# Kernel tuning notes

Measured on AMD Instinct MI355X. Metric: run time of the kernel, lower is better.

Reference implementation:

```python
import jax, jax.numpy as jnp
import numpy as np

TIME_WINDOW = 100  # init arg: time_window
RATIO = 1.0        # init arg: ratio


def setup_inputs() -> dict:
    key = jax.random.key(0)
    img = jax.random.uniform(key, (16, 1, 224, 224), dtype=jnp.float32)  # values in [0,1)
    return {"img": img}


def reference(img):
    T = TIME_WINDOW
    orig_shape = img.shape
    N = img.size
    flat = img.reshape(-1) * RATIO                      # [N]
    nz = flat != 0
    # rate = 1/(img*ratio) where nonzero, else 0 (Poisson(0) samples are always 0)
    lam = jnp.where(nz, 1.0 / jnp.where(nz, flat, 1.0), 0.0)
    key = jax.random.key(42)
    intervals = jax.random.poisson(key, lam, shape=(T, N)).astype(jnp.float32)  # [T, N]
    # for nonzero pixels, force a minimum inter-spike interval of 1 timestep
    intervals = jnp.where(nz[None, :] & (intervals == 0), 1.0, intervals)
    times = jnp.cumsum(intervals, axis=0).astype(jnp.int32)  # [T, N], spike times >= 1
    # times beyond the window collapse into row 0 (discarded below)
    times = jnp.where(times >= T + 1, 0, times)
    spikes = jnp.zeros((T + 1, N), dtype=bool)
    col = jnp.arange(N, dtype=jnp.int32)
    spikes = spikes.at[times, col[None, :]].set(True)   # scatter by computed times
    spikes = spikes[1:]                                  # drop the dump row 0
    return spikes.reshape((T,) + orig_shape)
```

## Files before the change

### kernel.cpp

```cpp
#include <hip/hip_runtime.h>
#include <math.h>
#include <stdint.h>

#pragma clang fp contract(off)

#define N_PIX 802816
#define T_WIN 100
#define KN_MAX 96
#define RJ_MAX 48
#define G_SLOT (KN_MAX * 2 + RJ_MAX * 4)
#define TAB_BASE 98000
#define TAB_N    4096
#define TAB_WS   (G_SLOT + 1)
#define WS_NEEDED ((TAB_WS + TAB_N) * 4)

__device__ __forceinline__ void tf2x32(uint32_t k0, uint32_t k1,
                                       uint32_t x0, uint32_t x1,
                                       uint32_t &o0, uint32_t &o1) {
  uint32_t ks2 = k0 ^ k1 ^ 0x1BD11BDAu;
  x0 += k0; x1 += k1;
#define TF_R(r) { x0 += x1; x1 = (x1 << (r)) | (x1 >> (32 - (r))); x1 ^= x0; }
  TF_R(13) TF_R(15) TF_R(26) TF_R(6)
  x0 += k1;  x1 += ks2 + 1u;
  TF_R(17) TF_R(29) TF_R(16) TF_R(24)
  x0 += ks2; x1 += k0 + 2u;
  TF_R(13) TF_R(15) TF_R(26) TF_R(6)
  x0 += k0;  x1 += k1 + 3u;
  TF_R(17) TF_R(29) TF_R(16) TF_R(24)
  x0 += k1;  x1 += ks2 + 4u;
  TF_R(13) TF_R(15) TF_R(26) TF_R(6)
  x0 += ks2; x1 += k0 + 5u;
#undef TF_R
  o0 = x0; o1 = x1;
}

__device__ __forceinline__ uint32_t unif_bits(uint32_t s0, uint32_t s1, uint32_t p) {
  uint32_t a, b;
  tf2x32(s0, s1, 0u, p, a, b);
  return a ^ b;
}

__device__ __forceinline__ float bits_to_unit(uint32_t bits) {
  return __uint_as_float(0x3f800000u | (bits >> 9)) - 1.0f;
}

__device__ __forceinline__ float xla_logf(float xin) {
#pragma clang fp contract(off)
  if (xin == 0.0f) return __uint_as_float(0xff800000u);
  if (!(xin > 0.0f)) return __uint_as_float(0x7fc00000u);
  float x = fmaxf(xin, __uint_as_float(0x00800000u));
  uint32_t ib = __float_as_uint(x);
  float e = (float)((int)(ib >> 23) - 126);
  ib = (ib & 0x007fffffu) | 0x3f000000u;
  x = __uint_as_float(ib);
  float tmp = 0.0f, eadj = 0.0f;
  if (x < (float)0.707106781186547524) { tmp = x; eadj = 1.0f; }
  x = x - 1.0f;
  e = e - eadj;
  x = x + tmp;
  float x2 = x * x;
  float x3 = x2 * x;
  float y  = fmaf((float)7.0376836292e-2,  x, (float)-1.1514610310e-1);
  float y1 = fmaf((float)-1.2420140846e-1, x, (float)1.4249322787e-1);
  float y2 = fmaf((float)2.0000714765e-1,  x, (float)-2.4999993993e-1);
  y  = fmaf(y,  x, (float)1.1676998740e-1);
  y1 = fmaf(y1, x, (float)-1.6668057665e-1);
  y2 = fmaf(y2, x, (float)3.3333331174e-1);
  y  = fmaf(y, x3, y1);
  y  = fmaf(y, x3, y2);
  float eq1 = e * (float)-2.12194440e-4;
  y = fmaf(y, x3, eq1);
  x = fmaf(-x2, 0.5f, x);
  x = x + y;
  x = fmaf(e, (float)0.693359375, x);
  return x;
}

__device__ __forceinline__ float xla_log1pf(float w) {
#pragma clang fp contract(off)
  if (fabsf(w) < (float)1e-4) return fmaf(-0.5f, w, 1.0f) * w;
  return xla_logf(w + 1.0f);
}

__device__ __forceinline__ float xla_lgammaf_pos(float x) {
#pragma clang fp contract(off)
  const float kBase = (float)0.99999999999980993227684700473478;
  const float c0 = (float)676.520368121885098567009190444019;
  const float c1 = (float)-1259.13921672240287047156078755283;
  const float c2 = (float)771.3234287776530788486528258894;
  const float c3 = (float)-176.61502916214059906584551354;
  const float c4 = (float)12.507343278686904814458936853;
  const float c5 = (float)-0.13857109526572011689554707;
  const float c6 = (float)9.984369578019570859563e-6;
  const float c7 = (float)1.50563273514931155834e-7;
  const float kLogSqrtTwoPi = (float)0.91893853320467274178032973640562;
  const float kGPlusHalf = 7.5f;
  const float kLogGPlusHalf = (float)2.0149030205422647065;
  float z = x - 1.0f;
  float sum = kBase;
  sum = sum + c0 / ((z + 0.0f) + 1.0f);
  sum = sum + c1 / ((z + 1.0f) + 1.0f);
  sum = sum + c2 / ((z + 2.0f) + 1.0f);
  sum = sum + c3 / ((z + 3.0f) + 1.0f);
  sum = sum + c4 / ((z + 4.0f) + 1.0f);
  sum = sum + c5 / ((z + 5.0f) + 1.0f);
  sum = sum + c6 / ((z + 6.0f) + 1.0f);
  sum = sum + c7 / ((z + 7.0f) + 1.0f);
  float t = kGPlusHalf + z;
  float log_t = kLogGPlusHalf + xla_log1pf(z / kGPlusHalf);
  float log_y = fmaf((z + 0.5f) - t / log_t, log_t, kLogSqrtTwoPi) + xla_logf(sum);
  return log_y;
}

struct RejConst {
  float lam, neg_lam, log_lam, aa, bb, inv_alpha, v_r, two_a;
};

__device__ __forceinline__ RejConst make_rej(float lam) {
  RejConst rc;
  rc.lam = lam;
  rc.neg_lam = -lam;
  rc.log_lam = xla_logf(lam);
  float sq = (float)sqrt((double)lam);
  rc.bb = fmaf(2.53f, sq, (float)0.931);
  rc.aa = fmaf((float)0.02483, rc.bb, (float)-0.059);
  rc.inv_alpha = (float)1.1239 + (float)1.1328 / (rc.bb - (float)3.4);
  rc.v_r = (float)0.9277 - (float)3.6224 / (rc.bb - 2.0f);
  rc.two_a = 2.0f * rc.aa;
  return rc;
}

__device__ __forceinline__ bool rej_step4(const RejConst& rc, uint4 ch,
                                          uint32_t p, float& kf_out) {
  float u = bits_to_unit(unif_bits(ch.x, ch.y, p)) - 0.5f;
  float v = bits_to_unit(unif_bits(ch.z, ch.w, p));
  float u_sh = 0.5f - fabsf(u);
  float kf = floorf(fmaf(rc.two_a / u_sh + rc.bb, u, rc.lam) + (float)0.43);
  kf_out = kf;
  if ((u_sh >= (float)0.07) && (v <= rc.v_r)) return true;
  if ((kf < 0.0f) || ((u_sh < (float)0.013) && (v > u_sh))) return false;
  float sv = xla_logf((v * rc.inv_alpha) / ((rc.aa / (u_sh * u_sh)) + rc.bb));
  float tv = fmaf(kf, rc.log_lam, rc.neg_lam) - xla_lgammaf_pos(kf + 1.0f);
  return sv <= tv;
}

__global__ void chain_init(uint32_t* __restrict__ ws, int build_table) {
  if (blockIdx.x == 0) {
    if (threadIdx.x != 0) return;
    ws[G_SLOT] = 0u;
    uint32_t r0 = 0u, r1 = 42u;
    for (int j = 0; j < KN_MAX; ++j) {
      uint32_t s0, s1, n0, n1;
      tf2x32(r0, r1, 0u, 1u, s0, s1);
      tf2x32(r0, r1, 0u, 0u, n0, n1);
      ws[2 * j] = s0; ws[2 * j + 1] = s1;
      r0 = n0; r1 = n1;
    }
  } else if (blockIdx.x == 1) {
    if (threadIdx.x != 0) return;
    uint32_t c0 = 0u, c1 = 42u;
    for (int j = 0; j < RJ_MAX; ++j) {
      uint32_t a0, a1, b0, b1, n0, n1;
      tf2x32(c0, c1, 0u, 1u, a0, a1);
      tf2x32(c0, c1, 0u, 2u, b0, b1);
      tf2x32(c0, c1, 0u, 0u, n0, n1);
      uint32_t base = KN_MAX * 2 + 4 * j;
      ws[base + 0] = a0; ws[base + 1] = a1; ws[base + 2] = b0; ws[base + 3] = b1;
      c0 = n0; c1 = n1;
    }
  } else if (build_table) {
    int i = (blockIdx.x - 2) * 256 + threadIdx.x;
    if (i < TAB_N) {
      float kf = (float)(TAB_BASE + i);
      ws[TAB_WS + i] = __float_as_uint(xla_lgammaf_pos(kf + 1.0f));
    }
  }
}

__global__ void __launch_bounds__(512)
rej_gmax(const float* __restrict__ img, const uint32_t* __restrict__ ws,
         uint32_t* __restrict__ gmax, int use_table) {
  __shared__ uint4 rj4[RJ_MAX];
  __shared__ float lgtab[TAB_N];
  __shared__ int waveRej[8];
  __shared__ unsigned short order[512];
  __shared__ uint32_t red[512];

  const int tid = threadIdx.x;
  for (int i = tid; i < RJ_MAX; i += 512) {
    uint32_t b = KN_MAX * 2 + 4 * i;
    rj4[i] = make_uint4(ws[b], ws[b + 1], ws[b + 2], ws[b + 3]);
  }
  if (use_table)
    for (int i = tid; i < TAB_N; i += 512) lgtab[i] = __uint_as_float(ws[TAB_WS + i]);

  int n0 = blockIdx.x * 512 + tid;
  float uimg0 = img[n0];
  bool isRej = (uimg0 != 0.0f) && !((1.0f / uimg0) < 10.0f);
  int lane = tid & 63, w = tid >> 6;
  unsigned long long bal = __ballot(isRej ? 1 : 0);
  int within = (int)__popcll(bal & ((1ull << lane) - 1ull));
  if (lane == 0) waveRej[w] = (int)__popcll(bal);
  __syncthreads();
  int rejBefore = 0, totalRej = 0;
  for (int i = 0; i < 8; ++i) { int c = waveRej[i]; totalRej += c; if (i < w) rejBefore += c; }
  int nMasked = 512 - totalRej;
  int slot = isRej ? (nMasked + rejBefore + within)
                   : (64 * w - rejBefore) + (lane - within);
  order[slot] = (unsigned short)tid;
  __syncthreads();

  int n = blockIdx.x * 512 + (int)order[tid];
  bool myRej = (tid >= nMasked);
  RejConst rc = make_rej(myRej ? (1.0f / img[n]) : 100000.0f);

  uint32_t mymax = 1;
  {
    uint32_t p = (uint32_t)n;
    int t = 0, j = 0;
    while (t < T_WIN) {
      uint4 ch = rj4[j];
      float u = bits_to_unit(unif_bits(ch.x, ch.y, p)) - 0.5f;
      float v = bits_to_unit(unif_bits(ch.z, ch.w, p));
      float u_sh = 0.5f - fabsf(u);
      float kf = floorf(fmaf(rc.two_a / u_sh + rc.bb, u, rc.lam) + (float)0.43);
      bool acc;
      if ((u_sh >= (float)0.07) && (v <= rc.v_r)) acc = true;
      else if ((kf < 0.0f) || ((u_sh < (float)0.013) && (v > u_sh))) acc = false;
      else {
        float sv = xla_logf((v * rc.inv_alpha) / ((rc.aa / (u_sh * u_sh)) + rc.bb));
        int ki = (int)kf - TAB_BASE;
        float lg;
        if (use_table && ki >= 0 && ki < TAB_N) lg = lgtab[ki];
        else lg = xla_lgammaf_pos(kf + 1.0f);
        float tv = fmaf(kf, rc.log_lam, rc.neg_lam) - lg;
        acc = (sv <= tv);
      }
      if (acc) {
        uint32_t fa = (uint32_t)(j + 1);
        if (fa > mymax) mymax = fa;
        ++t; p += N_PIX; j = 0;
      } else if (++j >= RJ_MAX) {
        mymax = RJ_MAX;
        ++t; p += N_PIX; j = 0;
      }
    }
  }
  red[tid] = mymax;
  __syncthreads();
  for (int s2 = 256; s2 > 0; s2 >>= 1) {
    if (tid < s2) {
      uint32_t o = red[tid + s2];
      if (o > red[tid]) red[tid] = o;
    }
    __syncthreads();
  }
  if (tid == 0) atomicMax((unsigned int*)gmax, red[0]);
}

__global__ void __launch_bounds__(512)
spike_main(const float* __restrict__ img, int* __restrict__ out,
           const uint32_t* __restrict__ chains) {
  __shared__ uint2 kn2[KN_MAX];
  __shared__ uint4 rj4[RJ_MAX];
  __shared__ int waveRej[8];
  __shared__ unsigned short order[512];
  __shared__ int shG;
  __shared__ ulonglong2 bmsh[512];

  const int tid = threadIdx.x;
  for (int i = tid; i < KN_MAX; i += 512)
    kn2[i] = make_uint2(chains[2 * i], chains[2 * i + 1]);
  for (int i = tid; i < RJ_MAX; i += 512) {
    uint32_t b = KN_MAX * 2 + 4 * i;
    rj4[i] = make_uint4(chains[b], chains[b + 1], chains[b + 2], chains[b + 3]);
  }
  if (tid == 0) shG = (int)chains[G_SLOT];

  int n0 = blockIdx.x * 512 + tid;
  float uimg0 = img[n0];
  bool isRej = (uimg0 != 0.0f) && !((1.0f / uimg0) < 10.0f);
  int lane = tid & 63, w = tid >> 6;
  unsigned long long bal = __ballot(isRej ? 1 : 0);
  int within = (int)__popcll(bal & ((1ull << lane) - 1ull));
  if (lane == 0) waveRej[w] = (int)__popcll(bal);
  __syncthreads();
  int rejBefore = 0, totalRej = 0;
  for (int i = 0; i < 8; ++i) { int c = waveRej[i]; totalRej += c; if (i < w) rejBefore += c; }
  int nMasked = 512 - totalRej;
  int slot = isRej ? (nMasked + rejBefore + within)
                   : (64 * w - rejBefore) + (lane - within);
  order[slot] = (unsigned short)tid;
  __syncthreads();

  const int G = shG;
  int nl = (int)order[tid];
  int n = blockIdx.x * 512 + nl;
  bool myRej = (tid >= nMasked);
  float uimg = img[n];
  unsigned long long bm0 = 0ull, bm1 = 0ull;

  if (myRej) {
    RejConst rc = make_rej(1.0f / uimg);
    uint32_t p = (uint32_t)n;
    int s = 0, j = G - 1, t = 0;
    while (t < T_WIN) {
      float kf;
      bool acc = rej_step4(rc, rj4[j], p, kf);
      if (acc) {
        int iv = (kf >= 102.0f) ? 102 : (int)kf;
        if (iv == 0) iv = 1;
        s += iv;
        if (s > T_WIN) break;
        if (s <= 64) bm0 |= 1ull << (s - 1); else bm1 |= 1ull << (s - 65);
        ++t; p += N_PIX; j = G - 1;
      } else if (--j < 0) {
        break;
      }
    }
  } else if (uimg != 0.0f) {
    float lam = 1.0f / uimg;
    float neg_lam = -lam;
    uint32_t p = (uint32_t)n;
    int s = 0, k = 0, j = 0;
    float lp = 0.0f;
    while (true) {
      uint2 sk = kn2[j];
      float u = bits_to_unit(unif_bits(sk.x, sk.y, p));
      ++k; ++j;
      lp = lp + xla_logf(u);
      if (lp <= neg_lam || j >= KN_MAX) {
        int iv = k - 1;
        if (iv == 0) iv = 1;
        s += iv;
        if (s > T_WIN) break;
        if (s <= 64) bm0 |= 1ull << (s - 1); else bm1 |= 1ull << (s - 65);
        p += N_PIX; j = 0; k = 0; lp = 0.0f;
        if (p >= (uint32_t)T_WIN * (uint32_t)N_PIX) break;
      }
    }
  }

  ulonglong2 bm; bm.x = bm0; bm.y = bm1;
  bmsh[nl] = bm;
  __syncthreads();
  ulonglong2 b2 = bmsh[tid];
  size_t base = (size_t)(blockIdx.x * 512 + tid);
  for (int t = 0; t < 64; ++t)
    out[base + (size_t)t * N_PIX] = (int)((b2.x >> t) & 1ull);
  for (int t = 64; t < T_WIN; ++t)
    out[base + (size_t)t * N_PIX] = (int)((b2.y >> (t - 64)) & 1ull);
}

extern "C" void kernel_launch(void* const* d_in, const int* in_sizes, int n_in,
                              void* d_out, int out_size, void* d_ws, size_t ws_size,
                              hipStream_t stream) {
  const float* img = (const float*)d_in[0];
  int* out = (int*)d_out;
  uint32_t* ws = (uint32_t*)d_ws;
  int use_table = (ws_size >= (size_t)WS_NEEDED) ? 1 : 0;
  hipLaunchKernelGGL(chain_init, dim3(2 + TAB_N / 256), dim3(256), 0, stream,
                     ws, use_table);
  hipLaunchKernelGGL(rej_gmax, dim3(N_PIX / 512), dim3(512), 0, stream,
                     img, ws, ws + G_SLOT, use_table);
  hipLaunchKernelGGL(spike_main, dim3(N_PIX / 512), dim3(512), 0, stream,
                     img, out, ws);
}
```

Baseline: 1.243 ms.

## Split rejection max-chain search into first-candidate pass plus compacted retry list

The single rej_gmax kernel becomes two stages. A first pass evaluates only the first rejection candidate for every pixel and timestep and appends the rejected (pixel, timestep) positions to a global list through wave-local buffers and atomics. A second kernel grid-strides over that list only, walking the rest of the chain to find the global maximum chain length. The old full kernel stays as a fallback that runs only on list overflow or when the workspace is too small. The aim is to remove the divergence and serial while-loop cost of the old per-pixel walk. In exchange it needs a 32 MB list, global atomics and two extra launches.

```diff
diff --git a/kernel.cpp b/kernel.cpp
--- a/kernel.cpp
+++ b/kernel.cpp
@@ -9,10 +9,17 @@
 #define KN_MAX 96
 #define RJ_MAX 48
 #define G_SLOT (KN_MAX * 2 + RJ_MAX * 4)
+#define MRC_WS (G_SLOT + 1)
+#define CNT_WS (MRC_WS + 8)
+#define OVF_WS (CNT_WS + 1)
 #define TAB_BASE 98000
 #define TAB_N    4096
-#define TAB_WS   (G_SLOT + 1)
-#define WS_NEEDED ((TAB_WS + TAB_N) * 4)
+#define TAB_WS   (OVF_WS + 1)
+#define LIST_WS  (TAB_WS + TAB_N)
+#define LIST_CAP (8u * 1024u * 1024u)
+#define WS_TAB_NEEDED ((size_t)(TAB_WS + TAB_N) * 4)
+#define WS_FAST_NEEDED ((size_t)(LIST_WS + LIST_CAP) * 4)
+#define WBUF 640
 
 __device__ __forceinline__ void tf2x32(uint32_t k0, uint32_t k1,
                                        uint32_t x0, uint32_t x1,
@@ -144,10 +151,28 @@
   return sv <= tv;
 }
 
-__global__ void chain_init(uint32_t* __restrict__ ws, int build_table) {
+__device__ __forceinline__ bool rej_step_tab(const RejConst& rc, uint4 ch,
+                                             uint32_t p, const float* lgtab,
+                                             float& kf_out) {
+  float u = bits_to_unit(unif_bits(ch.x, ch.y, p)) - 0.5f;
+  float v = bits_to_unit(unif_bits(ch.z, ch.w, p));
+  float u_sh = 0.5f - fabsf(u);
+  float kf = floorf(fmaf(rc.two_a / u_sh + rc.bb, u, rc.lam) + (float)0.43);
+  kf_out = kf;
+  if ((u_sh >= (float)0.07) && (v <= rc.v_r)) return true;
+  if ((kf < 0.0f) || ((u_sh < (float)0.013) && (v > u_sh))) return false;
+  float sv = xla_logf((v * rc.inv_alpha) / ((rc.aa / (u_sh * u_sh)) + rc.bb));
+  int ki = (int)kf - TAB_BASE;
+  float lg = (ki >= 0 && ki < TAB_N) ? lgtab[ki] : xla_lgammaf_pos(kf + 1.0f);
+  float tv = fmaf(kf, rc.log_lam, rc.neg_lam) - lg;
+  return sv <= tv;
+}
+
+__global__ void chain_init(uint32_t* __restrict__ ws, int build_table, int fast) {
   if (blockIdx.x == 0) {
     if (threadIdx.x != 0) return;
-    ws[G_SLOT] = 0u;
+    ws[G_SLOT] = 1u;
+    if (fast) { ws[CNT_WS] = 0u; ws[OVF_WS] = 0u; }
     uint32_t r0 = 0u, r1 = 42u;
     for (int j = 0; j < KN_MAX; ++j) {
       uint32_t s0, s1, n0, n1;
@@ -157,16 +182,27 @@
       r0 = n0; r1 = n1;
     }
   } else if (blockIdx.x == 1) {
-    if (threadIdx.x != 0) return;
-    uint32_t c0 = 0u, c1 = 42u;
-    for (int j = 0; j < RJ_MAX; ++j) {
-      uint32_t a0, a1, b0, b1, n0, n1;
-      tf2x32(c0, c1, 0u, 1u, a0, a1);
-      tf2x32(c0, c1, 0u, 2u, b0, b1);
-      tf2x32(c0, c1, 0u, 0u, n0, n1);
-      uint32_t base = KN_MAX * 2 + 4 * j;
-      ws[base + 0] = a0; ws[base + 1] = a1; ws[base + 2] = b0; ws[base + 3] = b1;
-      c0 = n0; c1 = n1;
+    if (threadIdx.x == 0) {
+      uint32_t c0 = 0u, c1 = 42u;
+      for (int j = 0; j < RJ_MAX; ++j) {
+        uint32_t a0, a1, b0, b1, n0, n1;
+        tf2x32(c0, c1, 0u, 1u, a0, a1);
+        tf2x32(c0, c1, 0u, 2u, b0, b1);
+        tf2x32(c0, c1, 0u, 0u, n0, n1);
+        uint32_t base = KN_MAX * 2 + 4 * j;
+        ws[base + 0] = a0; ws[base + 1] = a1; ws[base + 2] = b0; ws[base + 3] = b1;
+        c0 = n0; c1 = n1;
+      }
+    } else if (threadIdx.x == 64 && fast) {
+      RejConst m = make_rej(100000.0f);
+      ws[MRC_WS + 0] = __float_as_uint(m.lam);
+      ws[MRC_WS + 1] = __float_as_uint(m.neg_lam);
+      ws[MRC_WS + 2] = __float_as_uint(m.log_lam);
+      ws[MRC_WS + 3] = __float_as_uint(m.aa);
+      ws[MRC_WS + 4] = __float_as_uint(m.bb);
+      ws[MRC_WS + 5] = __float_as_uint(m.inv_alpha);
+      ws[MRC_WS + 6] = __float_as_uint(m.v_r);
+      ws[MRC_WS + 7] = __float_as_uint(m.two_a);
     }
   } else if (build_table) {
     int i = (blockIdx.x - 2) * 256 + threadIdx.x;
@@ -177,22 +213,25 @@
   }
 }
 
+__device__ __forceinline__ RejConst load_mrc(const float* mrcsh) {
+  RejConst rc;
+  rc.lam = mrcsh[0]; rc.neg_lam = mrcsh[1]; rc.log_lam = mrcsh[2];
+  rc.aa = mrcsh[3];  rc.bb = mrcsh[4];      rc.inv_alpha = mrcsh[5];
+  rc.v_r = mrcsh[6]; rc.two_a = mrcsh[7];
+  return rc;
+}
+
 __global__ void __launch_bounds__(512)
-rej_gmax(const float* __restrict__ img, const uint32_t* __restrict__ ws,
-         uint32_t* __restrict__ gmax, int use_table) {
-  __shared__ uint4 rj4[RJ_MAX];
+rej_pass0(const float* __restrict__ img, uint32_t* __restrict__ ws) {
   __shared__ float lgtab[TAB_N];
+  __shared__ float mrcsh[8];
   __shared__ int waveRej[8];
   __shared__ unsigned short order[512];
-  __shared__ uint32_t red[512];
+  __shared__ uint32_t wbuf[8][WBUF];
 
   const int tid = threadIdx.x;
-  for (int i = tid; i < RJ_MAX; i += 512) {
-    uint32_t b = KN_MAX * 2 + 4 * i;
-    rj4[i] = make_uint4(ws[b], ws[b + 1], ws[b + 2], ws[b + 3]);
-  }
-  if (use_table)
-    for (int i = tid; i < TAB_N; i += 512) lgtab[i] = __uint_as_float(ws[TAB_WS + i]);
+  for (int i = tid; i < TAB_N; i += 512) lgtab[i] = __uint_as_float(ws[TAB_WS + i]);
+  if (tid < 8) mrcsh[tid] = __uint_as_float(ws[MRC_WS + tid]);
 
   int n0 = blockIdx.x * 512 + tid;
   float uimg0 = img[n0];
@@ -212,6 +251,132 @@
 
   int n = blockIdx.x * 512 + (int)order[tid];
   bool myRej = (tid >= nMasked);
+  RejConst rc;
+  if (myRej) rc = make_rej(1.0f / img[n]);
+  else       rc = load_mrc(mrcsh);
+
+  uint4 ch0 = make_uint4(ws[KN_MAX * 2 + 0], ws[KN_MAX * 2 + 1],
+                         ws[KN_MAX * 2 + 2], ws[KN_MAX * 2 + 3]);
+  uint32_t* cnt  = ws + CNT_WS;
+  uint32_t* list = ws + LIST_WS;
+  uint32_t wcnt = 0;
+  uint32_t p = (uint32_t)n;
+
+  for (int t = 0; t < T_WIN; ++t, p += N_PIX) {
+    float kf;
+    bool acc = rej_step_tab(rc, ch0, p, lgtab, kf);
+    unsigned long long mask = __ballot(acc ? 0 : 1);
+    if (mask) {
+      uint32_t rank = (uint32_t)__popcll(mask & ((1ull << lane) - 1ull));
+      if (!acc) wbuf[w][wcnt + rank] = p;
+      wcnt += (uint32_t)__popcll(mask);
+    }
+    if (wcnt >= WBUF - 64) {
+      uint32_t base = 0;
+      if (lane == 0) base = atomicAdd(cnt, wcnt);
+      base = (uint32_t)__shfl((int)base, 0, 64);
+      for (uint32_t i = (uint32_t)lane; i < wcnt; i += 64) {
+        uint32_t idx = base + i;
+        if (idx < LIST_CAP) list[idx] = wbuf[w][i];
+        else atomicOr(ws + OVF_WS, 1u);
+      }
+      wcnt = 0;
+    }
+  }
+  if (wcnt > 0) {
+    uint32_t base = 0;
+    if (lane == 0) base = atomicAdd(cnt, wcnt);
+    base = (uint32_t)__shfl((int)base, 0, 64);
+    for (uint32_t i = (uint32_t)lane; i < wcnt; i += 64) {
+      uint32_t idx = base + i;
+      if (idx < LIST_CAP) list[idx] = wbuf[w][i];
+      else atomicOr(ws + OVF_WS, 1u);
+    }
+  }
+}
+
+__global__ void __launch_bounds__(256)
+rej_finish(const float* __restrict__ img, uint32_t* __restrict__ ws,
+           uint32_t* __restrict__ gmax) {
+  __shared__ uint4 rj4[RJ_MAX];
+  __shared__ float lgtab[TAB_N];
+  __shared__ float mrcsh[8];
+  __shared__ uint32_t red[256];
+  const int tid = threadIdx.x;
+  for (int i = tid; i < RJ_MAX; i += 256) {
+    uint32_t b = KN_MAX * 2 + 4 * i;
+    rj4[i] = make_uint4(ws[b], ws[b + 1], ws[b + 2], ws[b + 3]);
+  }
+  for (int i = tid; i < TAB_N; i += 256) lgtab[i] = __uint_as_float(ws[TAB_WS + i]);
+  if (tid < 8) mrcsh[tid] = __uint_as_float(ws[MRC_WS + tid]);
+  __syncthreads();
+
+  uint32_t cnt = ws[CNT_WS];
+  if (cnt > LIST_CAP) cnt = LIST_CAP;
+  uint32_t mymax = 1;
+  for (uint32_t i = blockIdx.x * 256 + tid; i < cnt; i += gridDim.x * 256) {
+    uint32_t p = ws[LIST_WS + i];
+    uint32_t n = p % (uint32_t)N_PIX;
+    float uimg = img[n];
+    bool isRej = (uimg != 0.0f) && !((1.0f / uimg) < 10.0f);
+    RejConst rc;
+    if (isRej) rc = make_rej(1.0f / uimg);
+    else       rc = load_mrc(mrcsh);
+    uint32_t fa = RJ_MAX;
+    for (int j = 1; j < RJ_MAX; ++j) {
+      float kf;
+      if (rej_step_tab(rc, rj4[j], p, lgtab, kf)) { fa = (uint32_t)(j + 1); break; }
+    }
+    if (fa > mymax) mymax = fa;
+  }
+  red[tid] = mymax;
+  __syncthreads();
+  for (int s2 = 128; s2 > 0; s2 >>= 1) {
+    if (tid < s2) {
+      uint32_t o = red[tid + s2];
+      if (o > red[tid]) red[tid] = o;
+    }
+    __syncthreads();
+  }
+  if (tid == 0) atomicMax((unsigned int*)gmax, red[0]);
+}
+
+__global__ void __launch_bounds__(512)
+rej_gmax_full(const float* __restrict__ img, const uint32_t* __restrict__ ws,
+              uint32_t* __restrict__ gmax, int use_table, int skip_unless_ovf) {
+  if (skip_unless_ovf && ws[OVF_WS] == 0u) return;
+  __shared__ uint4 rj4[RJ_MAX];
+  __shared__ float lgtab[TAB_N];
+  __shared__ int waveRej[8];
+  __shared__ unsigned short order[512];
+  __shared__ uint32_t red[512];
+
+  const int tid = threadIdx.x;
+  for (int i = tid; i < RJ_MAX; i += 512) {
+    uint32_t b = KN_MAX * 2 + 4 * i;
+    rj4[i] = make_uint4(ws[b], ws[b + 1], ws[b + 2], ws[b + 3]);
+  }
+  if (use_table)
+    for (int i = tid; i < TAB_N; i += 512) lgtab[i] = __uint_as_float(ws[TAB_WS + i]);
+
+  int n0 = blockIdx.x * 512 + tid;
+  float uimg0 = img[n0];
+  bool isRej = (uimg0 != 0.0f) && !((1.0f / uimg0) < 10.0f);
+  int lane = tid & 63, w = tid >> 6;
+  unsigned long long bal = __ballot(isRej ? 1 : 0);
+  int within = (int)__popcll(bal & ((1ull << lane) - 1ull));
+  if (lane == 0) waveRej[w] = (int)__popcll(bal);
+  __syncthreads();
+  int rejBefore = 0, totalRej = 0;
+  for (int i = 0; i < 8; ++i) { int c = waveRej[i]; totalRej += c; if (i < w) rejBefore += c; }
+  int nMasked = 512 - totalRej;
+  int slot = isRej ? (nMasked + rejBefore + within)
+                   : (64 * w - rejBefore) + (lane - within);
+  order[slot] = (unsigned short)tid;
+  __syncthreads();
+
+  int n = blockIdx.x * 512 + (int)order[tid];
+  bool myRej = (tid >= nMasked);
   RejConst rc = make_rej(myRej ? (1.0f / img[n]) : 100000.0f);
 
   uint32_t mymax = 1;
@@ -219,23 +384,10 @@
     uint32_t p = (uint32_t)n;
     int t = 0, j = 0;
     while (t < T_WIN) {
-      uint4 ch = rj4[j];
-      float u = bits_to_unit(unif_bits(ch.x, ch.y, p)) - 0.5f;
-      float v = bits_to_unit(unif_bits(ch.z, ch.w, p));
-      float u_sh = 0.5f - fabsf(u);
-      float kf = floorf(fmaf(rc.two_a / u_sh + rc.bb, u, rc.lam) + (float)0.43);
+      float kf;
       bool acc;
-      if ((u_sh >= (float)0.07) && (v <= rc.v_r)) acc = true;
-      else if ((kf < 0.0f) || ((u_sh < (float)0.013) && (v > u_sh))) acc = false;
-      else {
-        float sv = xla_logf((v * rc.inv_alpha) / ((rc.aa / (u_sh * u_sh)) + rc.bb));
-        int ki = (int)kf - TAB_BASE;
-        float lg;
-        if (use_table && ki >= 0 && ki < TAB_N) lg = lgtab[ki];
-        else lg = xla_lgammaf_pos(kf + 1.0f);
-        float tv = fmaf(kf, rc.log_lam, rc.neg_lam) - lg;
-        acc = (sv <= tv);
-      }
+      if (use_table) acc = rej_step_tab(rc, rj4[j], p, lgtab, kf);
+      else           acc = rej_step4(rc, rj4[j], p, kf);
       if (acc) {
         uint32_t fa = (uint32_t)(j + 1);
         if (fa > mymax) mymax = fa;
@@ -358,11 +510,18 @@
   const float* img = (const float*)d_in[0];
   int* out = (int*)d_out;
   uint32_t* ws = (uint32_t*)d_ws;
-  int use_table = (ws_size >= (size_t)WS_NEEDED) ? 1 : 0;
+  int use_table = (ws_size >= WS_TAB_NEEDED) ? 1 : 0;
+  int use_fast  = (use_table && ws_size >= WS_FAST_NEEDED) ? 1 : 0;
+
   hipLaunchKernelGGL(chain_init, dim3(2 + TAB_N / 256), dim3(256), 0, stream,
-                     ws, use_table);
-  hipLaunchKernelGGL(rej_gmax, dim3(N_PIX / 512), dim3(512), 0, stream,
-                     img, ws, ws + G_SLOT, use_table);
+                     ws, use_table, use_fast);
+  if (use_fast) {
+    hipLaunchKernelGGL(rej_pass0, dim3(N_PIX / 512), dim3(512), 0, stream, img, ws);
+    hipLaunchKernelGGL(rej_finish, dim3(512), dim3(256), 0, stream,
+                       img, ws, ws + G_SLOT);
+  }
+  hipLaunchKernelGGL(rej_gmax_full, dim3(N_PIX / 512), dim3(512), 0, stream,
+                     img, ws, ws + G_SLOT, use_table, use_fast);
   hipLaunchKernelGGL(spike_main, dim3(N_PIX / 512), dim3(512), 0, stream,
                      img, out, ws);
 }
```

Result: slower. 2.565 ms (+106.3%).

## Use persistent blocks with atomic chunk work-stealing for gmax and spike kernels

Applied to the files above, without the earlier changes.

Both the rejection-max kernel and the spike kernel become persistent grids of 1024 blocks that pull 512-pixel chunks from global atomic counters instead of one block per chunk. This is meant to balance the uneven per-chunk cost of rejection sampling and to amortize the per-block setup of the chain tables and lgamma LDS table. It adds an atomic plus two barriers per chunk and a fallback kernel for when the workspace is too small. The G slot now starts at 1 and is clamped.

```diff
diff --git a/kernel.cpp b/kernel.cpp
--- a/kernel.cpp
+++ b/kernel.cpp
@@ -8,11 +8,15 @@
 #define T_WIN 100
 #define KN_MAX 96
 #define RJ_MAX 48
-#define G_SLOT (KN_MAX * 2 + RJ_MAX * 4)
+#define N_CHUNK 1568
+
+#define G_SLOT 384
+#define CTR0_WS 385
+#define CTR1_WS 386
+#define TAB_WS  400
 #define TAB_BASE 98000
 #define TAB_N    4096
-#define TAB_WS   (G_SLOT + 1)
-#define WS_NEEDED ((TAB_WS + TAB_N) * 4)
+#define WS_TAB_NEEDED ((size_t)(TAB_WS + TAB_N) * 4)
 
 __device__ __forceinline__ void tf2x32(uint32_t k0, uint32_t k1,
                                        uint32_t x0, uint32_t x1,
@@ -144,10 +148,28 @@
   return sv <= tv;
 }
 
+__device__ __forceinline__ bool rej_step_lds(const RejConst& rc, uint4 ch,
+                                             uint32_t p, const float* lgtab,
+                                             float& kf_out) {
+  float u = bits_to_unit(unif_bits(ch.x, ch.y, p)) - 0.5f;
+  float v = bits_to_unit(unif_bits(ch.z, ch.w, p));
+  float u_sh = 0.5f - fabsf(u);
+  float kf = floorf(fmaf(rc.two_a / u_sh + rc.bb, u, rc.lam) + (float)0.43);
+  kf_out = kf;
+  if ((u_sh >= (float)0.07) && (v <= rc.v_r)) return true;
+  if ((kf < 0.0f) || ((u_sh < (float)0.013) && (v > u_sh))) return false;
+  float sv = xla_logf((v * rc.inv_alpha) / ((rc.aa / (u_sh * u_sh)) + rc.bb));
+  int ki = (int)kf - TAB_BASE;
+  float lg = (ki >= 0 && ki < TAB_N) ? lgtab[ki] : xla_lgammaf_pos(kf + 1.0f);
+  float tv = fmaf(kf, rc.log_lam, rc.neg_lam) - lg;
+  return sv <= tv;
+}
+
 __global__ void chain_init(uint32_t* __restrict__ ws, int build_table) {
   if (blockIdx.x == 0) {
     if (threadIdx.x != 0) return;
-    ws[G_SLOT] = 0u;
+    ws[G_SLOT] = 1u;
+    ws[CTR0_WS] = 0u; ws[CTR1_WS] = 0u;
     uint32_t r0 = 0u, r1 = 42u;
     for (int j = 0; j < KN_MAX; ++j) {
       uint32_t s0, s1, n0, n1;
@@ -178,64 +200,56 @@
 }
 
 __global__ void __launch_bounds__(512)
-rej_gmax(const float* __restrict__ img, const uint32_t* __restrict__ ws,
-         uint32_t* __restrict__ gmax, int use_table) {
+gmax_ws(const float* __restrict__ img, uint32_t* __restrict__ ws,
+        uint32_t* __restrict__ gmax) {
   __shared__ uint4 rj4[RJ_MAX];
   __shared__ float lgtab[TAB_N];
   __shared__ int waveRej[8];
   __shared__ unsigned short order[512];
   __shared__ uint32_t red[512];
+  __shared__ uint32_t curC;
 
   const int tid = threadIdx.x;
   for (int i = tid; i < RJ_MAX; i += 512) {
     uint32_t b = KN_MAX * 2 + 4 * i;
     rj4[i] = make_uint4(ws[b], ws[b + 1], ws[b + 2], ws[b + 3]);
   }
-  if (use_table)
-    for (int i = tid; i < TAB_N; i += 512) lgtab[i] = __uint_as_float(ws[TAB_WS + i]);
-
-  int n0 = blockIdx.x * 512 + tid;
-  float uimg0 = img[n0];
-  bool isRej = (uimg0 != 0.0f) && !((1.0f / uimg0) < 10.0f);
-  int lane = tid & 63, w = tid >> 6;
-  unsigned long long bal = __ballot(isRej ? 1 : 0);
-  int within = (int)__popcll(bal & ((1ull << lane) - 1ull));
-  if (lane == 0) waveRej[w] = (int)__popcll(bal);
-  __syncthreads();
-  int rejBefore = 0, totalRej = 0;
-  for (int i = 0; i < 8; ++i) { int c = waveRej[i]; totalRej += c; if (i < w) rejBefore += c; }
-  int nMasked = 512 - totalRej;
-  int slot = isRej ? (nMasked + rejBefore + within)
-                   : (64 * w - rejBefore) + (lane - within);
-  order[slot] = (unsigned short)tid;
-  __syncthreads();
-
-  int n = blockIdx.x * 512 + (int)order[tid];
-  bool myRej = (tid >= nMasked);
-  RejConst rc = make_rej(myRej ? (1.0f / img[n]) : 100000.0f);
+  for (int i = tid; i < TAB_N; i += 512)
+    lgtab[i] = __uint_as_float(ws[TAB_WS + i]);
 
   uint32_t mymax = 1;
-  {
+  while (true) {
+    __syncthreads();
+    if (tid == 0) curC = atomicAdd(ws + CTR0_WS, 1u);
+    __syncthreads();
+    uint32_t c = curC;
+    if (c >= (uint32_t)N_CHUNK) break;
+
+    int n0 = (int)c * 512 + tid;
+    float uimg0 = img[n0];
+    bool isRej = (uimg0 != 0.0f) && !((1.0f / uimg0) < 10.0f);
+    int lane = tid & 63, w = tid >> 6;
+    unsigned long long bal = __ballot(isRej ? 1 : 0);
+    int within = (int)__popcll(bal & ((1ull << lane) - 1ull));
+    if (lane == 0) waveRej[w] = (int)__popcll(bal);
+    __syncthreads();
+    int rejBefore = 0, totalRej = 0;
+    for (int i = 0; i < 8; ++i) { int cc = waveRej[i]; totalRej += cc; if (i < w) rejBefore += cc; }
+    int nMasked = 512 - totalRej;
+    int slot = isRej ? (nMasked + rejBefore + within)
+                     : (64 * w - rejBefore) + (lane - within);
+    order[slot] = (unsigned short)tid;
+    __syncthreads();
+
+    int n = (int)c * 512 + (int)order[tid];
+    bool myRej = (tid >= nMasked);
+    RejConst rc = make_rej(myRej ? (1.0f / img[n]) : 100000.0f);
+
     uint32_t p = (uint32_t)n;
     int t = 0, j = 0;
     while (t < T_WIN) {
-      uint4 ch = rj4[j];
-      float u = bits_to_unit(unif_bits(ch.x, ch.y, p)) - 0.5f;
-      float v = bits_to_unit(unif_bits(ch.z, ch.w, p));
-      float u_sh = 0.5f - fabsf(u);
-      float kf = floorf(fmaf(rc.two_a / u_sh + rc.bb, u, rc.lam) + (float)0.43);
-      bool acc;
-      if ((u_sh >= (float)0.07) && (v <= rc.v_r)) acc = true;
-      else if ((kf < 0.0f) || ((u_sh < (float)0.013) && (v > u_sh))) acc = false;
-      else {
-        float sv = xla_logf((v * rc.inv_alpha) / ((rc.aa / (u_sh * u_sh)) + rc.bb));
-        int ki = (int)kf - TAB_BASE;
-        float lg;
-        if (use_table && ki >= 0 && ki < TAB_N) lg = lgtab[ki];
-        else lg = xla_lgammaf_pos(kf + 1.0f);
-        float tv = fmaf(kf, rc.log_lam, rc.neg_lam) - lg;
-        acc = (sv <= tv);
-      }
+      float kf;
+      bool acc = rej_step_lds(rc, rj4[j], p, lgtab, kf);
       if (acc) {
         uint32_t fa = (uint32_t)(j + 1);
         if (fa > mymax) mymax = fa;
@@ -246,6 +260,7 @@
       }
     }
   }
+
   red[tid] = mymax;
   __syncthreads();
   for (int s2 = 256; s2 > 0; s2 >>= 1) {
@@ -259,14 +274,57 @@
 }
 
 __global__ void __launch_bounds__(512)
-spike_main(const float* __restrict__ img, int* __restrict__ out,
-           const uint32_t* __restrict__ chains) {
+rej_gmax_full(const float* __restrict__ img, const uint32_t* __restrict__ ws,
+              uint32_t* __restrict__ gmax) {
+  __shared__ uint4 rj4[RJ_MAX];
+  __shared__ uint32_t red[512];
+  const int tid = threadIdx.x;
+  for (int i = tid; i < RJ_MAX; i += 512) {
+    uint32_t b = KN_MAX * 2 + 4 * i;
+    rj4[i] = make_uint4(ws[b], ws[b + 1], ws[b + 2], ws[b + 3]);
+  }
+  __syncthreads();
+  int n = blockIdx.x * 512 + tid;
+  float uimg = img[n];
+  bool isRej = (uimg != 0.0f) && !((1.0f / uimg) < 10.0f);
+  RejConst rc = make_rej(isRej ? (1.0f / uimg) : 100000.0f);
+  uint32_t mymax = 1;
+  uint32_t p = (uint32_t)n;
+  int t = 0, j = 0;
+  while (t < T_WIN) {
+    float kf;
+    bool acc = rej_step4(rc, rj4[j], p, kf);
+    if (acc) {
+      uint32_t fa = (uint32_t)(j + 1);
+      if (fa > mymax) mymax = fa;
+      ++t; p += N_PIX; j = 0;
+    } else if (++j >= RJ_MAX) {
+      mymax = RJ_MAX;
+      ++t; p += N_PIX; j = 0;
+    }
+  }
+  red[tid] = mymax;
+  __syncthreads();
+  for (int s2 = 256; s2 > 0; s2 >>= 1) {
+    if (tid < s2) {
+      uint32_t o = red[tid + s2];
+      if (o > red[tid]) red[tid] = o;
+    }
+    __syncthreads();
+  }
+  if (tid == 0) atomicMax((unsigned int*)gmax, red[0]);
+}
+
+__global__ void __launch_bounds__(512)
+spike_ws(const float* __restrict__ img, int* __restrict__ out,
+         const uint32_t* __restrict__ chains, uint32_t* __restrict__ wsctr) {
   __shared__ uint2 kn2[KN_MAX];
   __shared__ uint4 rj4[RJ_MAX];
   __shared__ int waveRej[8];
   __shared__ unsigned short order[512];
   __shared__ int shG;
   __shared__ ulonglong2 bmsh[512];
+  __shared__ uint32_t curC;
 
   const int tid = threadIdx.x;
   for (int i = tid; i < KN_MAX; i += 512)
@@ -275,81 +333,94 @@
     uint32_t b = KN_MAX * 2 + 4 * i;
     rj4[i] = make_uint4(chains[b], chains[b + 1], chains[b + 2], chains[b + 3]);
   }
-  if (tid == 0) shG = (int)chains[G_SLOT];
-
-  int n0 = blockIdx.x * 512 + tid;
-  float uimg0 = img[n0];
-  bool isRej = (uimg0 != 0.0f) && !((1.0f / uimg0) < 10.0f);
-  int lane = tid & 63, w = tid >> 6;
-  unsigned long long bal = __ballot(isRej ? 1 : 0);
-  int within = (int)__popcll(bal & ((1ull << lane) - 1ull));
-  if (lane == 0) waveRej[w] = (int)__popcll(bal);
-  __syncthreads();
-  int rejBefore = 0, totalRej = 0;
-  for (int i = 0; i < 8; ++i) { int c = waveRej[i]; totalRej += c; if (i < w) rejBefore += c; }
-  int nMasked = 512 - totalRej;
-  int slot = isRej ? (nMasked + rejBefore + within)
-                   : (64 * w - rejBefore) + (lane - within);
-  order[slot] = (unsigned short)tid;
-  __syncthreads();
-
-  const int G = shG;
-  int nl = (int)order[tid];
-  int n = blockIdx.x * 512 + nl;
-  bool myRej = (tid >= nMasked);
-  float uimg = img[n];
-  unsigned long long bm0 = 0ull, bm1 = 0ull;
-
-  if (myRej) {
-    RejConst rc = make_rej(1.0f / uimg);
-    uint32_t p = (uint32_t)n;
-    int s = 0, j = G - 1, t = 0;
-    while (t < T_WIN) {
-      float kf;
-      bool acc = rej_step4(rc, rj4[j], p, kf);
-      if (acc) {
-        int iv = (kf >= 102.0f) ? 102 : (int)kf;
-        if (iv == 0) iv = 1;
-        s += iv;
-        if (s > T_WIN) break;
-        if (s <= 64) bm0 |= 1ull << (s - 1); else bm1 |= 1ull << (s - 65);
-        ++t; p += N_PIX; j = G - 1;
-      } else if (--j < 0) {
-        break;
+  if (tid == 0) {
+    int g = (int)chains[G_SLOT];
+    if (g < 1) g = 1;
+    if (g > RJ_MAX) g = RJ_MAX;
+    shG = g;
+  }
+
+  while (true) {
+    __syncthreads();
+    if (tid == 0) curC = atomicAdd(wsctr, 1u);
+    __syncthreads();
+    uint32_t c = curC;
+    if (c >= (uint32_t)N_CHUNK) break;
+
+    int n0 = (int)c * 512 + tid;
+    float uimg0 = img[n0];
+    bool isRej = (uimg0 != 0.0f) && !((1.0f / uimg0) < 10.0f);
+    int lane = tid & 63, w = tid >> 6;
+    unsigned long long bal = __ballot(isRej ? 1 : 0);
+    int within = (int)__popcll(bal & ((1ull << lane) - 1ull));
+    if (lane == 0) waveRej[w] = (int)__popcll(bal);
+    __syncthreads();
+    int rejBefore = 0, totalRej = 0;
+    for (int i = 0; i < 8; ++i) { int cc = waveRej[i]; totalRej += cc; if (i < w) rejBefore += cc; }
+    int nMasked = 512 - totalRej;
+    int slot = isRej ? (nMasked + rejBefore + within)
+                     : (64 * w - rejBefore) + (lane - within);
+    order[slot] = (unsigned short)tid;
+    __syncthreads();
+
+    const int G = shG;
+    int nl = (int)order[tid];
+    int n = (int)c * 512 + nl;
+    bool myRej = (tid >= nMasked);
+    float uimg = img[n];
+    unsigned long long bm0 = 0ull, bm1 = 0ull;
+
+    if (myRej) {
+      RejConst rc = make_rej(1.0f / uimg);
+      uint32_t p = (uint32_t)n;
+      int s = 0, j = G - 1, t = 0;
+      while (t < T_WIN) {
+        float kf;
+        bool acc = rej_step4(rc, rj4[j], p, kf);
+        if (acc) {
+          int iv = (kf >= 102.0f) ? 102 : (int)kf;
+          if (iv == 0) iv = 1;
+          s += iv;
+          if (s > T_WIN) break;
+          if (s <= 64) bm0 |= 1ull << (s - 1); else bm1 |= 1ull << (s - 65);
+          ++t; p += N_PIX; j = G - 1;
+        } else if (--j < 0) {
+          break;
+        }
       }
-    }
-  } else if (uimg != 0.0f) {
-    float lam = 1.0f / uimg;
-    float neg_lam = -lam;
-    uint32_t p = (uint32_t)n;
-    int s = 0, k = 0, j = 0;
-    float lp = 0.0f;
-    while (true) {
-      uint2 sk = kn2[j];
-      float u = bits_to_unit(unif_bits(sk.x, sk.y, p));
-      ++k; ++j;
-      lp = lp + xla_logf(u);
-      if (lp <= neg_lam || j >= KN_MAX) {
-        int iv = k - 1;
-        if (iv == 0) iv = 1;
-        s += iv;
-        if (s > T_WIN) break;
-        if (s <= 64) bm0 |= 1ull << (s - 1); else bm1 |= 1ull << (s - 65);
-        p += N_PIX; j = 0; k = 0; lp = 0.0f;
-        if (p >= (uint32_t)T_WIN * (uint32_t)N_PIX) break;
+    } else if (uimg != 0.0f) {
+      float lam = 1.0f / uimg;
+      float neg_lam = -lam;
+      uint32_t p = (uint32_t)n;
+      int s = 0, k = 0, j = 0;
+      float lp = 0.0f;
+      while (true) {
+        uint2 sk = kn2[j];
+        float u = bits_to_unit(unif_bits(sk.x, sk.y, p));
+        ++k; ++j;
+        lp = lp + xla_logf(u);
+        if (lp <= neg_lam || j >= KN_MAX) {
+          int iv = k - 1;
+          if (iv == 0) iv = 1;
+          s += iv;
+          if (s > T_WIN) break;
+          if (s <= 64) bm0 |= 1ull << (s - 1); else bm1 |= 1ull << (s - 65);
+          p += N_PIX; j = 0; k = 0; lp = 0.0f;
+          if (p >= (uint32_t)T_WIN * (uint32_t)N_PIX) break;
+        }
       }
     }
-  }
-
-  ulonglong2 bm; bm.x = bm0; bm.y = bm1;
-  bmsh[nl] = bm;
-  __syncthreads();
-  ulonglong2 b2 = bmsh[tid];
-  size_t base = (size_t)(blockIdx.x * 512 + tid);
-  for (int t = 0; t < 64; ++t)
-    out[base + (size_t)t * N_PIX] = (int)((b2.x >> t) & 1ull);
-  for (int t = 64; t < T_WIN; ++t)
-    out[base + (size_t)t * N_PIX] = (int)((b2.y >> (t - 64)) & 1ull);
+
+    ulonglong2 bm; bm.x = bm0; bm.y = bm1;
+    bmsh[nl] = bm;
+    __syncthreads();
+    ulonglong2 b2 = bmsh[tid];
+    size_t base = (size_t)((size_t)c * 512 + (size_t)tid);
+    for (int t = 0; t < 64; ++t)
+      out[base + (size_t)t * N_PIX] = (int)((b2.x >> t) & 1ull);
+    for (int t = 64; t < T_WIN; ++t)
+      out[base + (size_t)t * N_PIX] = (int)((b2.y >> (t - 64)) & 1ull);
+  }
 }
 
 extern "C" void kernel_launch(void* const* d_in, const int* in_sizes, int n_in,
@@ -358,11 +429,17 @@
   const float* img = (const float*)d_in[0];
   int* out = (int*)d_out;
   uint32_t* ws = (uint32_t*)d_ws;
-  int use_table = (ws_size >= (size_t)WS_NEEDED) ? 1 : 0;
+  int use_table = (ws_size >= WS_TAB_NEEDED) ? 1 : 0;
+
   hipLaunchKernelGGL(chain_init, dim3(2 + TAB_N / 256), dim3(256), 0, stream,
                      ws, use_table);
-  hipLaunchKernelGGL(rej_gmax, dim3(N_PIX / 512), dim3(512), 0, stream,
-                     img, ws, ws + G_SLOT, use_table);
-  hipLaunchKernelGGL(spike_main, dim3(N_PIX / 512), dim3(512), 0, stream,
-                     img, out, ws);
-}
+  if (use_table) {
+    hipLaunchKernelGGL(gmax_ws, dim3(1024), dim3(512), 0, stream,
+                       img, ws, ws + G_SLOT);
+  } else {
+    hipLaunchKernelGGL(rej_gmax_full, dim3(N_PIX / 512), dim3(512), 0, stream,
+                       img, ws, ws + G_SLOT);
+  }
+  hipLaunchKernelGGL(spike_ws, dim3(1024), dim3(512), 0, stream,
+                     img, out, ws, ws + CTR1_WS);
+}
```

New measurement: 1.257 ms. Within noise of the previous version (+1.1%).
